# Kernel optimization log

Hardware: AMD Instinct MI355X
Metric: run time of the kernel (lower is better)

The kernel has to match this reference:

```python
import jax, jax.numpy as jnp
import numpy as np

B, N, S, DIM, H = 128, 8, 16, 64, 4
DH = DIM // H

def setup_inputs() -> dict:
    key = jax.random.key(0)
    ks = jax.random.split(key, 10)
    return {
        "self_embeddings": jax.random.normal(ks[0], (B, N, DIM), jnp.float32),
        "ngh_user_embeddings": jax.random.normal(ks[1], (B, S, DIM), jnp.float32),
        "ngh_entity_embeddings": jax.random.normal(ks[2], (B, N, S, DIM), jnp.float32),
        "user_embeddings": jax.random.normal(ks[3], (B, DIM), jnp.float32),
        "item_embeddings": jax.random.normal(ks[4], (B, DIM), jnp.float32),
        "W_r": jax.random.normal(ks[5], (B, N, S, DIM, DIM), jnp.float32) * 0.1,
        "W_ui": jax.random.normal(ks[6], (DIM, DIM), jnp.float32) * 0.1,
        "lin_W": jax.random.normal(ks[7], (DIM, DIM), jnp.float32) * 0.1,
        "lin_b": jnp.zeros((DIM,), jnp.float32),
        "linUI_W": jax.random.normal(ks[8], (DIM, DIM), jnp.float32) * 0.1,
        "linUI_b": jnp.zeros((DIM,), jnp.float32),
        "is_item_layer": 1,
    }

def reference(self_embeddings, ngh_user_embeddings, ngh_entity_embeddings,
              user_embeddings, item_embeddings, W_r, W_ui,
              lin_W, lin_b, linUI_W, linUI_b, is_item_layer):
    scale = 1.0 / np.sqrt(float(DH))
    # ---- user-side ego embedding (agg_type='sum') ----
    # Wi[b,i] = sum_j W_ui[i,j] * item[b,j]
    Wi = item_embeddings @ W_ui.T                          # [B, DIM]
    Wi_h = Wi.reshape(B, H, DH)                            # split heads (chunks of DH)
    nghu_h = ngh_user_embeddings.reshape(B, S, H, DH)
    att_u = jnp.einsum('bhd,bshd->bhs', Wi_h, nghu_h) * scale
    att_u = jax.nn.softmax(att_u, axis=-1)                 # softmax over S
    user_ego = jnp.einsum('bhs,bshd->bhd', att_u, nghu_h).reshape(B, DIM)
    # sum-agg + linear_UI + act (dropout is identity at inference)
    item_UI = jax.nn.relu((item_embeddings + user_ego) @ linUI_W.T + linUI_b)  # [B, DIM]
    # ---- entity-side ego embedding (repr_type='sum') ----
    signal = user_embeddings + item_UI                     # [B, DIM]
    v = signal[:, None, :] * self_embeddings               # [B, N, DIM]
    # q[b,n,s,i] = sum_j W_r[b,n,s,i,j] * v[b,n,j]
    q = jnp.einsum('bnsij,bnj->bnsi', W_r, v)              # [B, N, S, DIM]
    q_h = q.reshape(B, N, S, H, DH)
    nghe_h = ngh_entity_embeddings.reshape(B, N, S, H, DH)
    att_e = jnp.einsum('bnshd,bnshd->bnhs', q_h, nghe_h) * scale
    att_e = jax.nn.softmax(att_e, axis=-1)                 # softmax over S
    entity_ego = jnp.einsum('bnhs,bnshd->bnhd', att_e, nghe_h).reshape(B, N, DIM)
    # ---- final aggregation (is_item_layer=True, agg_type='sum') ----
    agg = self_embeddings + user_ego[:, None, :] + entity_ego
    out = jax.nn.relu(agg @ lin_W.T + lin_b)               # [B, N, DIM]
    return out
```

## Files before the change

kernel.cpp:

```cpp
#include <hip/hip_runtime.h>
#include <hip/hip_bf16.h>

#define B_   128
#define N_   8
#define S_   16
#define DIM_ 64
#define H_   4
#define DH_  16

__device__ __forceinline__ float dot_row64f(const float* __restrict__ row,
                                            const float* __restrict__ v) {
    const float4* rp = (const float4*)row;
    float acc = 0.f;
#pragma unroll
    for (int m = 0; m < 16; ++m) {
        float4 u = rp[m];
        acc = fmaf(u.x, v[4 * m + 0], acc);
        acc = fmaf(u.y, v[4 * m + 1], acc);
        acc = fmaf(u.z, v[4 * m + 2], acc);
        acc = fmaf(u.w, v[4 * m + 3], acc);
    }
    return acc;
}

__device__ __forceinline__ void load_lds16(const float* g, float* lds) {
    __builtin_amdgcn_global_load_lds(
        (const __attribute__((address_space(1))) void*)g,
        (__attribute__((address_space(3))) void*)lds,
        16, 0, 0);
}

__global__ __launch_bounds__(256) void EntityAggregator_63342177681721_kernel(
    const float* __restrict__ self_e,
    const float* __restrict__ nghu,
    const float* __restrict__ nghe,
    const float* __restrict__ user_e,
    const float* __restrict__ item_e,
    const float* __restrict__ W_r,
    const float* __restrict__ W_ui,
    const float* __restrict__ lin_W,
    const float* __restrict__ lin_b,
    const float* __restrict__ linUI_W,
    const float* __restrict__ linUI_b,
    float* __restrict__ out)
{
    const int blk  = blockIdx.x;
    const int b    = blk >> 3;
    const int t    = threadIdx.x;
    const int w    = t >> 6;
    const int lane = t & 63;

    __shared__ __align__(16) float sW0[128 * DIM_];
    __shared__ __align__(16) float sW1[128 * DIM_];
    __shared__ float sU[S_][DIM_ + 1];
    __shared__ float sE[S_][DIM_ + 1];
    __shared__ float sQ[S_][DIM_ + 1];
    __shared__ float sItem[DIM_];
    __shared__ float sWi[DIM_];
    __shared__ float sAtt[H_][S_];
    __shared__ float sUei[DIM_];
    __shared__ float sTi[DIM_];
    __shared__ __align__(16) float sV[DIM_];
    __shared__ float sAgg[DIM_];

    const float* Wp = W_r + (size_t)blk * (S_ * DIM_ * DIM_);

    {
        const float* g0 = Wp + w * 256 + lane * 4;
#pragma unroll
        for (int rr = 0; rr < 8; ++rr)
            load_lds16(g0 + rr * 1024, sW0 + w * 256 + rr * 1024);
        const float* g1 = Wp + 8192 + w * 256 + lane * 4;
#pragma unroll
        for (int rr = 0; rr < 8; ++rr)
            load_lds16(g1 + rr * 1024, sW1 + w * 256 + rr * 1024);
    }

    {
        const int e0 = t * 4;
        const int s  = e0 >> 6;
        const int c  = e0 & 63;
        float4 uu = *(const float4*)(nghu + (size_t)b * S_ * DIM_ + e0);
        sU[s][c + 0] = uu.x; sU[s][c + 1] = uu.y;
        sU[s][c + 2] = uu.z; sU[s][c + 3] = uu.w;
        float4 ee = *(const float4*)(nghe + (size_t)blk * S_ * DIM_ + e0);
        sE[s][c + 0] = ee.x; sE[s][c + 1] = ee.y;
        sE[s][c + 2] = ee.z; sE[s][c + 3] = ee.w;
        if (t < DIM_) sItem[t] = item_e[(size_t)b * DIM_ + t];
    }
    __syncthreads();

    if (t < DIM_) sWi[t] = dot_row64f(W_ui + t * DIM_, sItem);
    __syncthreads();

    if (t < DIM_) {
        const int h = t >> 4, s = t & 15;
        float l = 0.f;
#pragma unroll
        for (int d = 0; d < DH_; ++d) l = fmaf(sWi[h * DH_ + d], sU[s][h * DH_ + d], l);
        l *= 0.25f;
        float mx = l;
#pragma unroll
        for (int off = 8; off; off >>= 1) mx = fmaxf(mx, __shfl_xor(mx, off, 16));
        float e = __expf(l - mx);
        float sm = e;
#pragma unroll
        for (int off = 8; off; off >>= 1) sm += __shfl_xor(sm, off, 16);
        sAtt[h][s] = e / sm;
    }
    __syncthreads();

    if (t < DIM_) {
        const int h = t >> 4;
        float ego = 0.f;
#pragma unroll
        for (int s = 0; s < S_; ++s) ego = fmaf(sAtt[h][s], sU[s][t], ego);
        sUei[t] = ego;
        sTi[t]  = sItem[t] + ego;
    }
    __syncthreads();

    if (t < DIM_) {
        float a   = dot_row64f(linUI_W + t * DIM_, sTi) + linUI_b[t];
        float iui = fmaxf(a, 0.f);
        float sig = user_e[(size_t)b * DIM_ + t] + iui;
        sV[t] = sig * self_e[(size_t)blk * DIM_ + t];
    }
    __syncthreads();

    {
        const int  row  = t >> 1;
        const int  half = t & 1;
        const float4* vv4 = (const float4*)sV;
#pragma unroll 1
        for (int c = 0; c < 8; ++c) {
            if (c >= 1 && c < 7) {
                float* nb = ((c + 1) & 1) ? sW1 : sW0;
                const float* g = Wp + (size_t)(c + 1) * 8192 + w * 256 + lane * 4;
#pragma unroll
                for (int rr = 0; rr < 8; ++rr)
                    load_lds16(g + rr * 1024, nb + w * 256 + rr * 1024);
            }
            const float4* bp = (const float4*)((c & 1) ? sW1 : sW0);
            float acc = 0.f;
#pragma unroll
            for (int m = 0; m < 8; ++m) {
                const int mm   = (m + row) & 7;
                const int col4 = half * 8 + mm;
                float4 u = bp[row * 16 + col4];
                float4 v = vv4[col4];
                acc = fmaf(u.x, v.x, acc);
                acc = fmaf(u.y, v.y, acc);
                acc = fmaf(u.z, v.z, acc);
                acc = fmaf(u.w, v.w, acc);
            }
            acc += __shfl_xor(acc, 1);
            if (half == 0) {
                const int rg = c * 128 + row;
                sQ[rg >> 6][rg & 63] = acc;
            }
            __syncthreads();
        }
    }

    if (t < DIM_) {
        const int h = t >> 4, s = t & 15;
        float l = 0.f;
#pragma unroll
        for (int d = 0; d < DH_; ++d) l = fmaf(sQ[s][h * DH_ + d], sE[s][h * DH_ + d], l);
        l *= 0.25f;
        float mx = l;
#pragma unroll
        for (int off = 8; off; off >>= 1) mx = fmaxf(mx, __shfl_xor(mx, off, 16));
        float e = __expf(l - mx);
        float sm = e;
#pragma unroll
        for (int off = 8; off; off >>= 1) sm += __shfl_xor(sm, off, 16);
        sAtt[h][s] = e / sm;
    }
    __syncthreads();

    if (t < DIM_) {
        const int h = t >> 4;
        float ego = 0.f;
#pragma unroll
        for (int s = 0; s < S_; ++s) ego = fmaf(sAtt[h][s], sE[s][t], ego);
        sAgg[t] = self_e[(size_t)blk * DIM_ + t] + sUei[t] + ego;
    }
    __syncthreads();

    if (t < DIM_) {
        float o = dot_row64f(lin_W + t * DIM_, sAgg) + lin_b[t];
        o = fmaxf(o, 0.f);
        out[(size_t)blk * DIM_ + t] = o;
    }
}

extern "C" void kernel_launch(void* const* d_in, const int* in_sizes, int n_in,
                              void* d_out, int out_size, void* d_ws, size_t ws_size,
                              hipStream_t stream) {
    (void)in_sizes; (void)n_in; (void)d_ws; (void)ws_size; (void)out_size;
    const float* self_e  = (const float*)d_in[0];
    const float* nghu    = (const float*)d_in[1];
    const float* nghe    = (const float*)d_in[2];
    const float* user_e  = (const float*)d_in[3];
    const float* item_e  = (const float*)d_in[4];
    const float* W_r     = (const float*)d_in[5];
    const float* W_ui    = (const float*)d_in[6];
    const float* lin_W   = (const float*)d_in[7];
    const float* lin_b   = (const float*)d_in[8];
    const float* linUI_W = (const float*)d_in[9];
    const float* linUI_b = (const float*)d_in[10];

    dim3 grid(B_ * N_);
    dim3 block(256);
    hipLaunchKernelGGL(EntityAggregator_63342177681721_kernel, grid, block, 0, stream,
                       self_e, nghu, nghe, user_e, item_e, W_r, W_ui,
                       lin_W, lin_b, linUI_W, linUI_b, (float*)d_out);
}
```

Before: 380.6 us.

## Give each wave private W_r double buffers and drop per-chunk block barriers

Each wave now streams its own contiguous quarter of the W_r slab into a private double-buffered LDS region. Waits use explicit s_waitcnt vmcnt counts instead of block-wide __syncthreads after every chunk, so waves run independently and prefetch the next chunk while computing the current one. The prefetch now covers all chunks rather than starting at the second. This relies on global_load_lds completion being tracked by vmcnt within a wave, and on each wave reading only the LDS data it loaded itself.

```diff
diff --git a/kernel.cpp b/kernel.cpp
--- a/kernel.cpp
+++ b/kernel.cpp
@@ -50,8 +50,7 @@
     const int w    = t >> 6;
     const int lane = t & 63;
 
-    __shared__ __align__(16) float sW0[128 * DIM_];
-    __shared__ __align__(16) float sW1[128 * DIM_];
+    __shared__ __align__(16) float sW[4 * 2 * 2048];
     __shared__ float sU[S_][DIM_ + 1];
     __shared__ float sE[S_][DIM_ + 1];
     __shared__ float sQ[S_][DIM_ + 1];
@@ -66,14 +65,11 @@
     const float* Wp = W_r + (size_t)blk * (S_ * DIM_ * DIM_);
 
     {
-        const float* g0 = Wp + w * 256 + lane * 4;
+        const float* g = Wp + w * 16384 + lane * 4;
+        float* l = sW + (w << 1) * 2048;
 #pragma unroll
         for (int rr = 0; rr < 8; ++rr)
-            load_lds16(g0 + rr * 1024, sW0 + w * 256 + rr * 1024);
-        const float* g1 = Wp + 8192 + w * 256 + lane * 4;
-#pragma unroll
-        for (int rr = 0; rr < 8; ++rr)
-            load_lds16(g1 + rr * 1024, sW1 + w * 256 + rr * 1024);
+            load_lds16(g + rr * 256, l + rr * 256);
     }
 
     {
@@ -129,25 +125,27 @@
     __syncthreads();
 
     {
-        const int  row  = t >> 1;
-        const int  half = t & 1;
+        const int r    = lane >> 1;
+        const int half = lane & 1;
         const float4* vv4 = (const float4*)sV;
 #pragma unroll 1
         for (int c = 0; c < 8; ++c) {
-            if (c >= 1 && c < 7) {
-                float* nb = ((c + 1) & 1) ? sW1 : sW0;
-                const float* g = Wp + (size_t)(c + 1) * 8192 + w * 256 + lane * 4;
+            if (c < 7) {
+                const float* g = Wp + w * 16384 + (c + 1) * 2048 + lane * 4;
+                float* lb = sW + (((w << 1) | ((c + 1) & 1))) * 2048;
 #pragma unroll
                 for (int rr = 0; rr < 8; ++rr)
-                    load_lds16(g + rr * 1024, nb + w * 256 + rr * 1024);
+                    load_lds16(g + rr * 256, lb + rr * 256);
+                asm volatile("s_waitcnt vmcnt(8)" ::: "memory");
+            } else {
+                asm volatile("s_waitcnt vmcnt(0)" ::: "memory");
             }
-            const float4* bp = (const float4*)((c & 1) ? sW1 : sW0);
+            const float4* bp = (const float4*)(sW + (((w << 1) | (c & 1))) * 2048);
             float acc = 0.f;
 #pragma unroll
             for (int m = 0; m < 8; ++m) {
-                const int mm   = (m + row) & 7;
-                const int col4 = half * 8 + mm;
-                float4 u = bp[row * 16 + col4];
+                const int col4 = half * 8 + ((m + r) & 7);
+                float4 u = bp[r * 16 + col4];
                 float4 v = vv4[col4];
                 acc = fmaf(u.x, v.x, acc);
                 acc = fmaf(u.y, v.y, acc);
@@ -156,12 +154,12 @@
             }
             acc += __shfl_xor(acc, 1);
             if (half == 0) {
-                const int rg = c * 128 + row;
-                sQ[rg >> 6][rg & 63] = acc;
+                const int rowg = w * 256 + c * 32 + r;
+                sQ[rowg >> 6][rowg & 63] = acc;
             }
-            __syncthreads();
         }
     }
+    __syncthreads();
 
     if (t < DIM_) {
         const int h = t >> 4, s = t & 15;
```

After: 380.5 us. No clear change (-0.0%).
